# Optimization experiments

Hardware: AMD Instinct MI355X
Metric: run time of the kernel (lower is better)

Reference implementation:

```python
import jax, jax.numpy as jnp
import numpy as np

S, B, H = 2048, 4, 1024

def setup_inputs() -> dict:
    key = jax.random.key(0)
    ks = jax.random.split(key, 9)
    s = 1.0 / np.sqrt(H)
    return {
        "x": jax.random.normal(ks[0], (S, B, H), jnp.float32),
        "ssm": jax.random.normal(ks[1], (B, S, S), jnp.float32),
        "Wq": jax.random.uniform(ks[2], (H, H), jnp.float32, -s, s),
        "bq": jax.random.uniform(ks[3], (H,), jnp.float32, -s, s),
        "Wk": jax.random.uniform(ks[4], (H, H), jnp.float32, -s, s),
        "bk": jax.random.uniform(ks[5], (H,), jnp.float32, -s, s),
        "Wv": jax.random.uniform(ks[6], (H, H), jnp.float32, -s, s),
        "bv": jax.random.uniform(ks[7], (H,), jnp.float32, -s, s),
        "beta": jnp.array(1.0, jnp.float32),
    }

def reference(x, ssm, Wq, bq, Wk, bk, Wv, bv, beta):
    scale = x.shape[-1] ** 0.5
    # projections on [S,B,H], then move to [B,S,H]
    Q = jnp.einsum('sbh,oh->bso', x, Wq) + bq
    K = jnp.einsum('sbh,oh->bso', x, Wk) + bk
    V = jnp.einsum('sbh,oh->bso', x, Wv) + bv
    scores = jnp.einsum('bqh,bkh->bqk', Q, K) / scale + beta * ssm
    attn = jax.nn.softmax(scores, axis=-1)
    out = jnp.einsum('bqk,bkh->bqh', attn, V)  # [B,S,H]
    return out.transpose(1, 0, 2)  # [S,B,H]
```

## Files before the change

kernel.cpp:

```cpp
#include <hip/hip_runtime.h>
#include <stdint.h>


#define S_LEN 2048
#define BATCH 4
#define HDIM  1024

typedef unsigned short u16;
typedef float f32x4  __attribute__((ext_vector_type(4)));
typedef short bf16x8 __attribute__((ext_vector_type(8)));
typedef u16   u16x4  __attribute__((ext_vector_type(4)));

__device__ __forceinline__ u16 f2bf(float f) {
  union { float f; uint32_t u; } c; c.f = f;
  uint32_t u = c.u;
  u += 0x7fffu + ((u >> 16) & 1u);
  return (u16)(u >> 16);
}

__global__ __launch_bounds__(256) void cast_f32_bf16(const float* __restrict__ src,
                                                     u16* __restrict__ dst, int n4) {
  int i = blockIdx.x * 256 + threadIdx.x;
  if (i >= n4) return;
  f32x4 v = *(const f32x4*)(src + (size_t)i * 4);
  u16x4 o;
  o.x = f2bf(v.x); o.y = f2bf(v.y); o.z = f2bf(v.z); o.w = f2bf(v.w);
  *(u16x4*)(dst + (size_t)i * 4) = o;
}

template <int MODE>
__global__ __launch_bounds__(256)
void gemm_bt(const u16* __restrict__ A, int lda, long bsA,
             const u16* __restrict__ Bm, int ldb, long bsB,
             void* __restrict__ Cp, int ldc, long bsC,
             int K,
             const float* __restrict__ E, int ldE, long bsE,
             const float* __restrict__ beta_p, float scale) {
  __shared__ u16 lA[128 * 64];
  __shared__ u16 lB[128 * 64];
  const int t = threadIdx.x;
  const int lane = t & 63;
  const int wave = t >> 6;
  const int wm = wave & 1, wn = wave >> 1;
  const int z = blockIdx.z;
  A  += (size_t)z * (size_t)bsA;
  Bm += (size_t)z * (size_t)bsB;
  const size_t brow = (size_t)blockIdx.x * 128;
  const size_t bcol = (size_t)blockIdx.y * 128;

  f32x4 acc[4][4] = {};

  int rowT[4], scT[4];
#pragma unroll
  for (int j = 0; j < 4; ++j) {
    int o = j * 4096 + t * 16;
    int row = o >> 7;
    int ch = (o >> 4) & 7;
    rowT[j] = row;
    scT[j] = (ch ^ (row & 7)) * 8;
  }
  const int ldsw = wave * 512;

  const u16* pA[4];
  const u16* pB[4];
#pragma unroll
  for (int j = 0; j < 4; ++j) {
    pA[j] = A  + (brow + rowT[j]) * (size_t)lda + scT[j];
    pB[j] = Bm + (bcol + rowT[j]) * (size_t)ldb + scT[j];
  }

  int offA[2][4], offB[2][4];
#pragma unroll
  for (int ks = 0; ks < 2; ++ks) {
#pragma unroll
    for (int i = 0; i < 4; ++i) {
      int ra = wm * 64 + i * 16 + (lane & 15);
      int rb = wn * 64 + i * 16 + (lane & 15);
      int c = ks * 4 + (lane >> 4);
      offA[ks][i] = ra * 64 + ((c ^ (ra & 7)) * 8);
      offB[ks][i] = rb * 64 + ((c ^ (rb & 7)) * 8);
    }
  }

  for (int k0 = 0; k0 < K; k0 += 64) {
    if (k0) __syncthreads();
#pragma unroll
    for (int j = 0; j < 4; ++j)
      __builtin_amdgcn_global_load_lds(
          (const __attribute__((address_space(1))) void*)(pA[j] + k0),
          (__attribute__((address_space(3))) void*)(lA + j * 2048 + ldsw), 16, 0, 0);
#pragma unroll
    for (int j = 0; j < 4; ++j)
      __builtin_amdgcn_global_load_lds(
          (const __attribute__((address_space(1))) void*)(pB[j] + k0),
          (__attribute__((address_space(3))) void*)(lB + j * 2048 + ldsw), 16, 0, 0);
    __syncthreads();

#pragma unroll
    for (int ks = 0; ks < 2; ++ks) {
      bf16x8 af[4], bf_[4];
#pragma unroll
      for (int mi = 0; mi < 4; ++mi) af[mi] = *(const bf16x8*)(lA + offA[ks][mi]);
#pragma unroll
      for (int ni = 0; ni < 4; ++ni) bf_[ni] = *(const bf16x8*)(lB + offB[ks][ni]);
#pragma unroll
      for (int mi = 0; mi < 4; ++mi)
#pragma unroll
        for (int ni = 0; ni < 4; ++ni)
          acc[mi][ni] = __builtin_amdgcn_mfma_f32_16x16x32_bf16(af[mi], bf_[ni],
                                                                acc[mi][ni], 0, 0, 0);
    }
  }

  const int r0 = (int)brow + wm * 64 + ((lane >> 4) << 2);
  const int c0 = (int)bcol + wn * 64 + (lane & 15);
  if constexpr (MODE == 0) {
    u16* C = (u16*)Cp;
#pragma unroll
    for (int ni = 0; ni < 4; ++ni) {
      int cc = c0 + ni * 16;
      float bv = E[cc];
#pragma unroll
      for (int mi = 0; mi < 4; ++mi)
#pragma unroll
        for (int q = 0; q < 4; ++q)
          C[(size_t)(r0 + mi * 16 + q) * ldc + cc] = f2bf((acc[mi][ni][q] + bv) * scale);
    }
  } else if constexpr (MODE == 1) {
    float* C = (float*)Cp + (size_t)z * (size_t)bsC;
    const float* Ez = E + (size_t)z * (size_t)bsE;
    const float beta = *beta_p;
#pragma unroll
    for (int ni = 0; ni < 4; ++ni) {
      int cc = c0 + ni * 16;
#pragma unroll
      for (int mi = 0; mi < 4; ++mi)
#pragma unroll
        for (int q = 0; q < 4; ++q) {
          int rr = r0 + mi * 16 + q;
          C[(size_t)rr * ldc + cc] = acc[mi][ni][q] + beta * Ez[(size_t)rr * ldE + cc];
        }
    }
  } else {
    float* C = (float*)Cp + (size_t)z * (size_t)bsC;
#pragma unroll
    for (int ni = 0; ni < 4; ++ni) {
      int cc = c0 + ni * 16;
#pragma unroll
      for (int mi = 0; mi < 4; ++mi)
#pragma unroll
        for (int q = 0; q < 4; ++q)
          C[(size_t)(r0 + mi * 16 + q) * ldc + cc] = acc[mi][ni][q];
    }
  }
}

__global__ __launch_bounds__(256) void transpose_v(const u16* __restrict__ V,
                                                   u16* __restrict__ Vt) {
  __shared__ u16 tile[64][68];
  const int b = blockIdx.z;
  const int s0 = blockIdx.x << 6, h0 = blockIdx.y << 6;
  const int t = threadIdx.x;
#pragma unroll
  for (int i = 0; i < 4; ++i) {
    int sl = (t >> 4) + i * 16;
    int hq = (t & 15) << 2;
    u16x4 v = *(const u16x4*)&V[((size_t)(s0 + sl) * BATCH + b) * HDIM + h0 + hq];
    *(u16x4*)&tile[sl][hq] = v;
  }
  __syncthreads();
#pragma unroll
  for (int i = 0; i < 4; ++i) {
    int hl = (t >> 4) + i * 16;
    int sq = (t & 15) << 2;
    u16x4 v;
    v.x = tile[sq + 0][hl]; v.y = tile[sq + 1][hl];
    v.z = tile[sq + 2][hl]; v.w = tile[sq + 3][hl];
    *(u16x4*)&Vt[((size_t)b * HDIM + h0 + hl) * S_LEN + s0 + sq] = v;
  }
}

__global__ __launch_bounds__(256) void softmax_row(float* __restrict__ scores) {
  const size_t row = blockIdx.x;
  float* rp = scores + row * 2048;
  const int t = threadIdx.x;
  const int lane = t & 63, wave = t >> 6;
  f32x4 v0 = *(const f32x4*)(rp + t * 8);
  f32x4 v1 = *(const f32x4*)(rp + t * 8 + 4);
  float m = -3.0e38f;
#pragma unroll
  for (int i = 0; i < 4; ++i) m = fmaxf(m, fmaxf(v0[i], v1[i]));
#pragma unroll
  for (int off = 32; off > 0; off >>= 1) m = fmaxf(m, __shfl_xor(m, off));
  __shared__ float red[8];
  if (lane == 0) red[wave] = m;
  __syncthreads();
  m = fmaxf(fmaxf(red[0], red[1]), fmaxf(red[2], red[3]));
  float e[8], s = 0.f;
#pragma unroll
  for (int i = 0; i < 4; ++i) { e[i] = __expf(v0[i] - m); s += e[i]; }
#pragma unroll
  for (int i = 0; i < 4; ++i) { e[4 + i] = __expf(v1[i] - m); s += e[4 + i]; }
#pragma unroll
  for (int off = 32; off > 0; off >>= 1) s += __shfl_xor(s, off);
  if (lane == 0) red[4 + wave] = s;
  __syncthreads();
  s = (red[4] + red[5]) + (red[6] + red[7]);
  const float inv = 1.0f / s;
  u16* wp = (u16*)rp;
  u16x4 o0, o1;
  o0.x = f2bf(e[0] * inv); o0.y = f2bf(e[1] * inv);
  o0.z = f2bf(e[2] * inv); o0.w = f2bf(e[3] * inv);
  o1.x = f2bf(e[4] * inv); o1.y = f2bf(e[5] * inv);
  o1.z = f2bf(e[6] * inv); o1.w = f2bf(e[7] * inv);
  *(u16x4*)(wp + t * 8) = o0;
  *(u16x4*)(wp + t * 8 + 4) = o1;
}

extern "C" void kernel_launch(void* const* d_in, const int* in_sizes, int n_in,
                              void* d_out, int out_size, void* d_ws, size_t ws_size,
                              hipStream_t stream) {
  const float* x    = (const float*)d_in[0];
  const float* ssm  = (const float*)d_in[1];
  const float* Wq   = (const float*)d_in[2];
  const float* bq   = (const float*)d_in[3];
  const float* Wk   = (const float*)d_in[4];
  const float* bk   = (const float*)d_in[5];
  const float* Wv   = (const float*)d_in[6];
  const float* bv   = (const float*)d_in[7];
  const float* beta = (const float*)d_in[8];
  float* out = (float*)d_out;

  char* p = (char*)d_ws;
  u16* xb  = (u16*)p; p += (size_t)8192 * 1024 * 2;
  u16* wqb = (u16*)p; p += (size_t)1024 * 1024 * 2;
  u16* wkb = (u16*)p; p += (size_t)1024 * 1024 * 2;
  u16* wvb = (u16*)p; p += (size_t)1024 * 1024 * 2;
  u16* Qs  = (u16*)p; p += (size_t)8192 * 1024 * 2;
  u16* Kb  = (u16*)p; p += (size_t)8192 * 1024 * 2;
  u16* Vb  = (u16*)p; p += (size_t)8192 * 1024 * 2;
  u16* Vt  = (u16*)p; p += (size_t)BATCH * HDIM * S_LEN * 2;
  float* sc = (float*)p;

  cast_f32_bf16<<<8192, 256, 0, stream>>>(x, xb, 2097152);
  cast_f32_bf16<<<1024, 256, 0, stream>>>(Wq, wqb, 262144);
  cast_f32_bf16<<<1024, 256, 0, stream>>>(Wk, wkb, 262144);
  cast_f32_bf16<<<1024, 256, 0, stream>>>(Wv, wvb, 262144);

  dim3 gp(64, 8, 1);
  gemm_bt<0><<<gp, 256, 0, stream>>>(xb, 1024, 0, wqb, 1024, 0, Qs, 1024, 0, 1024,
                                     bq, 0, 0, nullptr, 0.03125f);
  gemm_bt<0><<<gp, 256, 0, stream>>>(xb, 1024, 0, wkb, 1024, 0, Kb, 1024, 0, 1024,
                                     bk, 0, 0, nullptr, 1.0f);
  gemm_bt<0><<<gp, 256, 0, stream>>>(xb, 1024, 0, wvb, 1024, 0, Vb, 1024, 0, 1024,
                                     bv, 0, 0, nullptr, 1.0f);

  transpose_v<<<dim3(32, 16, 4), 256, 0, stream>>>(Vb, Vt);

  dim3 gs(16, 16, 4);
  gemm_bt<1><<<gs, 256, 0, stream>>>(Qs, 4096, 1024, Kb, 4096, 1024,
                                     sc, 2048, (long)2048 * 2048, 1024,
                                     ssm, 2048, (long)2048 * 2048, beta, 1.0f);

  softmax_row<<<8192, 256, 0, stream>>>(sc);

  dim3 gv(16, 8, 4);
  gemm_bt<2><<<gv, 256, 0, stream>>>((const u16*)sc, 4096, 8388608,
                                     Vt, 2048, (long)HDIM * S_LEN,
                                     out, 4096, 1024, 2048,
                                     nullptr, 0, 0, nullptr, 1.0f);
}
```

Before: 333.5 us.

## Fuse QKV projections into one 256x256-tile pipelined GEMM and reuse it for scores

Concatenates Wq/Wk/Wv and the biases so a single GEMM produces an interleaved QKV buffer. It adds a new 256x256-tile, 512-thread GEMM that double-buffers LDS and splits each k-step into four MFMA quadrants with barriers and raised priority, overlapping global-to-LDS loads with compute. The same kernel computes the scores GEMM, with the 1/sqrt(H) scale moved from the Q projection to the epilogue. The aim is fewer launches, more data reuse per tile and better load/compute overlap, at the cost of 128KB of LDS per block and a fragile hand-written wait/barrier schedule.

After: 383.2 us. +14.9%, slower.

```diff
diff --git a/kernel.cpp b/kernel.cpp
--- a/kernel.cpp
+++ b/kernel.cpp
@@ -26,6 +26,149 @@
   u16x4 o;
   o.x = f2bf(v.x); o.y = f2bf(v.y); o.z = f2bf(v.z); o.w = f2bf(v.w);
   *(u16x4*)(dst + (size_t)i * 4) = o;
+}
+
+__global__ __launch_bounds__(256) void pack_bias(const float* __restrict__ bq,
+                                                 const float* __restrict__ bk,
+                                                 const float* __restrict__ bv,
+                                                 float* __restrict__ bb) {
+  int i = blockIdx.x * 256 + threadIdx.x;
+  if (i < 1024) bb[i] = bq[i];
+  else if (i < 2048) bb[i] = bk[i - 1024];
+  else if (i < 3072) bb[i] = bv[i - 2048];
+}
+
+#define AS1 __attribute__((address_space(1)))
+#define AS3 __attribute__((address_space(3)))
+
+template <int MODE>
+__global__ __launch_bounds__(512, 2)
+void gemm256(const u16* __restrict__ A, int lda, long bsA,
+             const u16* __restrict__ Bm, int ldb, long bsB,
+             void* __restrict__ Cp, int ldc, long bsC,
+             int K,
+             const float* __restrict__ E, int ldE, long bsE,
+             const float* __restrict__ beta_p, float scale) {
+  __shared__ u16 lds[65536];
+  const int t = threadIdx.x;
+  const int lane = t & 63, wave = t >> 6;
+  const int wm = wave >> 2, wn = wave & 3;
+  const int z = blockIdx.z;
+  A  += (size_t)z * (size_t)bsA;
+  Bm += (size_t)z * (size_t)bsB;
+  const size_t brow = (size_t)blockIdx.x * 256;
+  const size_t bcol = (size_t)blockIdx.y * 256;
+  const int NT = K >> 6;
+
+  const int l8 = lane >> 3, l7 = lane & 7;
+  const int srow = wave * 8 + l8;
+  const int scol = (l7 ^ l8) * 8;
+  const u16* gA = A  + (size_t)(brow + srow) * lda + scol;
+  const u16* gB = Bm + (size_t)(bcol + srow) * ldb + scol;
+
+  const int fr = lane & 15, fc = lane >> 4;
+  int roff[2];
+  roff[0] = fr * 64 + ((0 * 4 + fc) ^ l7) * 8;
+  roff[1] = fr * 64 + ((1 * 4 + fc) ^ l7) * 8;
+
+  f32x4 acc[8][4] = {};
+  bf16x8 Af[4][2];
+  bf16x8 Bf[2][2][2];
+
+#define STAGE_A(kt, buf, q) __builtin_amdgcn_global_load_lds( \
+    (const AS1 void*)(gA + (size_t)(q) * 64 * lda + (size_t)(kt) * 64), \
+    (AS3 void*)(lds + (buf) * 32768 + (q) * 4096 + wave * 512), 16, 0, 0)
+#define STAGE_B(kt, buf, q) __builtin_amdgcn_global_load_lds( \
+    (const AS1 void*)(gB + (size_t)(q) * 64 * ldb + (size_t)(kt) * 64), \
+    (AS3 void*)(lds + (buf) * 32768 + 16384 + (q) * 4096 + wave * 512), 16, 0, 0)
+#define READ_A(mh) { _Pragma("unroll") for (int mi = 0; mi < 4; ++mi) { \
+    _Pragma("unroll") for (int ks = 0; ks < 2; ++ks) \
+      Af[mi][ks] = *(const bf16x8*)(LA + (wm * 128 + (mh) * 64 + mi * 16) * 64 + roff[ks]); } }
+#define READ_B(nh) { _Pragma("unroll") for (int ni = 0; ni < 2; ++ni) { \
+    _Pragma("unroll") for (int ks = 0; ks < 2; ++ks) \
+      Bf[nh][ni][ks] = *(const bf16x8*)(LB + (wn * 64 + (nh) * 32 + ni * 16) * 64 + roff[ks]); } }
+#define MFMA_Q(mh, nh) { _Pragma("unroll") for (int mi = 0; mi < 4; ++mi) { \
+    _Pragma("unroll") for (int ni = 0; ni < 2; ++ni) { \
+      _Pragma("unroll") for (int ks = 0; ks < 2; ++ks) \
+        acc[(mh) * 4 + mi][(nh) * 2 + ni] = __builtin_amdgcn_mfma_f32_16x16x32_bf16( \
+            Af[mi][ks], Bf[nh][ni][ks], acc[(mh) * 4 + mi][(nh) * 2 + ni], 0, 0, 0); } } }
+#define BAR() __builtin_amdgcn_s_barrier()
+#define LGKM0() asm volatile("s_waitcnt lgkmcnt(0)" ::: "memory")
+
+#pragma unroll
+  for (int q = 0; q < 4; ++q) STAGE_A(0, 0, q);
+#pragma unroll
+  for (int q = 0; q < 4; ++q) STAGE_B(0, 0, q);
+  STAGE_A(1, 1, 0); STAGE_A(1, 1, 2); STAGE_B(1, 1, 0); STAGE_B(1, 1, 1);
+  asm volatile("s_waitcnt vmcnt(4)" ::: "memory");
+  BAR();
+
+  int cur = 0;
+  for (int kt = 0; kt < NT; ++kt) {
+    const u16* LA = lds + cur * 32768;
+    const u16* LB = LA + 16384;
+    const int nxt = cur ^ 1;
+    READ_A(0); READ_B(0);
+    if (kt + 1 < NT) { STAGE_A(kt + 1, nxt, 1); STAGE_A(kt + 1, nxt, 3);
+                       STAGE_B(kt + 1, nxt, 2); STAGE_B(kt + 1, nxt, 3); }
+    BAR(); LGKM0();
+    __builtin_amdgcn_s_setprio(1); MFMA_Q(0, 0); __builtin_amdgcn_s_setprio(0);
+    BAR();
+    READ_B(1);
+    BAR(); LGKM0();
+    __builtin_amdgcn_s_setprio(1); MFMA_Q(0, 1); __builtin_amdgcn_s_setprio(0);
+    BAR();
+    READ_A(1);
+    if (kt + 2 < NT) { STAGE_A(kt + 2, cur, 0); STAGE_A(kt + 2, cur, 2); }
+    BAR(); LGKM0();
+    __builtin_amdgcn_s_setprio(1); MFMA_Q(1, 0); __builtin_amdgcn_s_setprio(0);
+    BAR();
+    if (kt + 2 < NT) { STAGE_B(kt + 2, cur, 0); STAGE_B(kt + 2, cur, 1); }
+    BAR(); LGKM0();
+    __builtin_amdgcn_s_setprio(1); MFMA_Q(1, 1); __builtin_amdgcn_s_setprio(0);
+    if (kt + 2 < NT) { asm volatile("s_waitcnt vmcnt(4)" ::: "memory"); }
+    else             { asm volatile("s_waitcnt vmcnt(0)" ::: "memory"); }
+    BAR();
+    cur = nxt;
+  }
+
+  const int r0 = (int)brow + wm * 128 + fc * 4;
+  const int c0 = (int)bcol + wn * 64 + fr;
+  if constexpr (MODE == 0) {
+    u16* C = (u16*)Cp;
+#pragma unroll
+    for (int nf = 0; nf < 4; ++nf) {
+      int cc = c0 + nf * 16;
+      float bv = E[cc];
+#pragma unroll
+      for (int mf = 0; mf < 8; ++mf)
+#pragma unroll
+        for (int q = 0; q < 4; ++q)
+          C[(size_t)(r0 + mf * 16 + q) * ldc + cc] = f2bf(acc[mf][nf][q] + bv);
+    }
+  } else {
+    float* C = (float*)Cp + (size_t)z * (size_t)bsC;
+    const float* Ez = E + (size_t)z * (size_t)bsE;
+    const float beta = *beta_p;
+#pragma unroll
+    for (int nf = 0; nf < 4; ++nf) {
+      int cc = c0 + nf * 16;
+#pragma unroll
+      for (int mf = 0; mf < 8; ++mf)
+#pragma unroll
+        for (int q = 0; q < 4; ++q) {
+          int rr = r0 + mf * 16 + q;
+          C[(size_t)rr * ldc + cc] = acc[mf][nf][q] * scale + beta * Ez[(size_t)rr * ldE + cc];
+        }
+    }
+  }
+#undef STAGE_A
+#undef STAGE_B
+#undef READ_A
+#undef READ_B
+#undef MFMA_Q
+#undef BAR
+#undef LGKM0
 }
 
 template <int MODE>
@@ -87,13 +230,13 @@
 #pragma unroll
     for (int j = 0; j < 4; ++j)
       __builtin_amdgcn_global_load_lds(
-          (const __attribute__((address_space(1))) void*)(pA[j] + k0),
-          (__attribute__((address_space(3))) void*)(lA + j * 2048 + ldsw), 16, 0, 0);
+          (const AS1 void*)(pA[j] + k0),
+          (AS3 void*)(lA + j * 2048 + ldsw), 16, 0, 0);
 #pragma unroll
     for (int j = 0; j < 4; ++j)
       __builtin_amdgcn_global_load_lds(
-          (const __attribute__((address_space(1))) void*)(pB[j] + k0),
-          (__attribute__((address_space(3))) void*)(lB + j * 2048 + ldsw), 16, 0, 0);
+          (const AS1 void*)(pB[j] + k0),
+          (AS3 void*)(lB + j * 2048 + ldsw), 16, 0, 0);
     __syncthreads();
 
 #pragma unroll
@@ -114,38 +257,11 @@
 
   const int r0 = (int)brow + wm * 64 + ((lane >> 4) << 2);
   const int c0 = (int)bcol + wn * 64 + (lane & 15);
-  if constexpr (MODE == 0) {
-    u16* C = (u16*)Cp;
+  {
+    float* C = (float*)Cp + (size_t)z * (size_t)bsC;
 #pragma unroll
     for (int ni = 0; ni < 4; ++ni) {
       int cc = c0 + ni * 16;
-      float bv = E[cc];
-#pragma unroll
-      for (int mi = 0; mi < 4; ++mi)
-#pragma unroll
-        for (int q = 0; q < 4; ++q)
-          C[(size_t)(r0 + mi * 16 + q) * ldc + cc] = f2bf((acc[mi][ni][q] + bv) * scale);
-    }
-  } else if constexpr (MODE == 1) {
-    float* C = (float*)Cp + (size_t)z * (size_t)bsC;
-    const float* Ez = E + (size_t)z * (size_t)bsE;
-    const float beta = *beta_p;
-#pragma unroll
-    for (int ni = 0; ni < 4; ++ni) {
-      int cc = c0 + ni * 16;
-#pragma unroll
-      for (int mi = 0; mi < 4; ++mi)
-#pragma unroll
-        for (int q = 0; q < 4; ++q) {
-          int rr = r0 + mi * 16 + q;
-          C[(size_t)rr * ldc + cc] = acc[mi][ni][q] + beta * Ez[(size_t)rr * ldE + cc];
-        }
-    }
-  } else {
-    float* C = (float*)Cp + (size_t)z * (size_t)bsC;
-#pragma unroll
-    for (int ni = 0; ni < 4; ++ni) {
-      int cc = c0 + ni * 16;
 #pragma unroll
       for (int mi = 0; mi < 4; ++mi)
 #pragma unroll
@@ -155,7 +271,7 @@
   }
 }
 
-__global__ __launch_bounds__(256) void transpose_v(const u16* __restrict__ V,
+__global__ __launch_bounds__(256) void transpose_v(const u16* __restrict__ QKV,
                                                    u16* __restrict__ Vt) {
   __shared__ u16 tile[64][68];
   const int b = blockIdx.z;
@@ -165,7 +281,7 @@
   for (int i = 0; i < 4; ++i) {
     int sl = (t >> 4) + i * 16;
     int hq = (t & 15) << 2;
-    u16x4 v = *(const u16x4*)&V[((size_t)(s0 + sl) * BATCH + b) * HDIM + h0 + hq];
+    u16x4 v = *(const u16x4*)&QKV[((size_t)(s0 + sl) * BATCH + b) * 3072 + 2048 + h0 + hq];
     *(u16x4*)&tile[sl][hq] = v;
   }
   __syncthreads();
@@ -233,34 +349,29 @@
 
   char* p = (char*)d_ws;
   u16* xb  = (u16*)p; p += (size_t)8192 * 1024 * 2;
-  u16* wqb = (u16*)p; p += (size_t)1024 * 1024 * 2;
-  u16* wkb = (u16*)p; p += (size_t)1024 * 1024 * 2;
-  u16* wvb = (u16*)p; p += (size_t)1024 * 1024 * 2;
-  u16* Qs  = (u16*)p; p += (size_t)8192 * 1024 * 2;
-  u16* Kb  = (u16*)p; p += (size_t)8192 * 1024 * 2;
-  u16* Vb  = (u16*)p; p += (size_t)8192 * 1024 * 2;
+  u16* wb  = (u16*)p; p += (size_t)3072 * 1024 * 2;
+  float* bb = (float*)p; p += 3072 * 4;
+  u16* QKV = (u16*)p; p += (size_t)8192 * 3072 * 2;
   u16* Vt  = (u16*)p; p += (size_t)BATCH * HDIM * S_LEN * 2;
   float* sc = (float*)p;
 
   cast_f32_bf16<<<8192, 256, 0, stream>>>(x, xb, 2097152);
-  cast_f32_bf16<<<1024, 256, 0, stream>>>(Wq, wqb, 262144);
-  cast_f32_bf16<<<1024, 256, 0, stream>>>(Wk, wkb, 262144);
-  cast_f32_bf16<<<1024, 256, 0, stream>>>(Wv, wvb, 262144);
-
-  dim3 gp(64, 8, 1);
-  gemm_bt<0><<<gp, 256, 0, stream>>>(xb, 1024, 0, wqb, 1024, 0, Qs, 1024, 0, 1024,
-                                     bq, 0, 0, nullptr, 0.03125f);
-  gemm_bt<0><<<gp, 256, 0, stream>>>(xb, 1024, 0, wkb, 1024, 0, Kb, 1024, 0, 1024,
-                                     bk, 0, 0, nullptr, 1.0f);
-  gemm_bt<0><<<gp, 256, 0, stream>>>(xb, 1024, 0, wvb, 1024, 0, Vb, 1024, 0, 1024,
-                                     bv, 0, 0, nullptr, 1.0f);
-
-  transpose_v<<<dim3(32, 16, 4), 256, 0, stream>>>(Vb, Vt);
-
-  dim3 gs(16, 16, 4);
-  gemm_bt<1><<<gs, 256, 0, stream>>>(Qs, 4096, 1024, Kb, 4096, 1024,
-                                     sc, 2048, (long)2048 * 2048, 1024,
-                                     ssm, 2048, (long)2048 * 2048, beta, 1.0f);
+  cast_f32_bf16<<<1024, 256, 0, stream>>>(Wq, wb, 262144);
+  cast_f32_bf16<<<1024, 256, 0, stream>>>(Wk, wb + 1024 * 1024, 262144);
+  cast_f32_bf16<<<1024, 256, 0, stream>>>(Wv, wb + 2048 * 1024, 262144);
+  pack_bias<<<12, 256, 0, stream>>>(bq, bk, bv, bb);
+
+  gemm256<0><<<dim3(32, 12, 1), 512, 0, stream>>>(xb, 1024, 0, wb, 1024, 0,
+                                                  QKV, 3072, 0, 1024,
+                                                  bb, 0, 0, nullptr, 1.0f);
+
+  transpose_v<<<dim3(32, 16, 4), 256, 0, stream>>>(QKV, Vt);
+
+  gemm256<1><<<dim3(8, 8, 4), 512, 0, stream>>>(QKV, 12288, 3072,
+                                                QKV + 1024, 12288, 3072,
+                                                sc, 2048, (long)2048 * 2048, 1024,
+                                                ssm, 2048, (long)2048 * 2048,
+                                                beta, 0.03125f);
 
   softmax_row<<<8192, 256, 0, stream>>>(sc);
 
```

## Fuse QKV projections into one GEMM, merge casts, add XCD-aware block remap

Applied to the files above, without the earlier changes.

Merges the four cast kernels into one launch that also packs the biases, and concatenates Wq/Wk/Wv so a single GEMM writes an interleaved QKV buffer. The Q scaling moves from the projection epilogue into the scores epilogue. All GEMMs now use a 1D grid with a swizzle that spreads consecutive tiles across the eight XCDs for better L2 locality. This cuts launch count and gives one larger projection GEMM, at the cost of a wider stride (3072) in the later reads of Q, K and V.

Result: slower. 341.6 us (+2.4%).

```diff
diff --git a/kernel.cpp b/kernel.cpp
--- a/kernel.cpp
+++ b/kernel.cpp
@@ -10,6 +10,9 @@
 typedef float f32x4  __attribute__((ext_vector_type(4)));
 typedef short bf16x8 __attribute__((ext_vector_type(8)));
 typedef u16   u16x4  __attribute__((ext_vector_type(4)));
+
+#define AS1 __attribute__((address_space(1)))
+#define AS3 __attribute__((address_space(3)))
 
 __device__ __forceinline__ u16 f2bf(float f) {
   union { float f; uint32_t u; } c; c.f = f;
@@ -18,14 +21,31 @@
   return (u16)(u >> 16);
 }
 
-__global__ __launch_bounds__(256) void cast_f32_bf16(const float* __restrict__ src,
-                                                     u16* __restrict__ dst, int n4) {
+__global__ __launch_bounds__(256)
+void cast_all(const float* __restrict__ x,
+              const float* __restrict__ Wq, const float* __restrict__ Wk,
+              const float* __restrict__ Wv,
+              const float* __restrict__ bq, const float* __restrict__ bk,
+              const float* __restrict__ bv,
+              u16* __restrict__ xb, u16* __restrict__ wb, float* __restrict__ bb) {
   int i = blockIdx.x * 256 + threadIdx.x;
-  if (i >= n4) return;
-  f32x4 v = *(const f32x4*)(src + (size_t)i * 4);
+  const float* src;
+  u16* dst;
+  if (i < 2097152) { src = x + (size_t)i * 4; dst = xb + (size_t)i * 4; }
+  else if (i < 2359296) { int j = i - 2097152; src = Wq + (size_t)j * 4; dst = wb + (size_t)j * 4; }
+  else if (i < 2621440) { int j = i - 2359296; src = Wk + (size_t)j * 4; dst = wb + 1048576 + (size_t)j * 4; }
+  else if (i < 2883584) { int j = i - 2621440; src = Wv + (size_t)j * 4; dst = wb + 2097152 + (size_t)j * 4; }
+  else {
+    int j = i - 2883584;
+    const float* s = (j < 256) ? bq : (j < 512) ? bk : bv;
+    int o = ((j < 256) ? j : (j < 512) ? j - 256 : j - 512) * 4;
+    *(f32x4*)(bb + j * 4) = *(const f32x4*)(s + o);
+    return;
+  }
+  f32x4 v = *(const f32x4*)src;
   u16x4 o;
   o.x = f2bf(v.x); o.y = f2bf(v.y); o.z = f2bf(v.z); o.w = f2bf(v.w);
-  *(u16x4*)(dst + (size_t)i * 4) = o;
+  *(u16x4*)dst = o;
 }
 
 template <int MODE>
@@ -35,18 +55,25 @@
              void* __restrict__ Cp, int ldc, long bsC,
              int K,
              const float* __restrict__ E, int ldE, long bsE,
-             const float* __restrict__ beta_p, float scale) {
+             const float* __restrict__ beta_p, float scale,
+             int gx, int gy) {
   __shared__ u16 lA[128 * 64];
   __shared__ u16 lB[128 * 64];
   const int t = threadIdx.x;
   const int lane = t & 63;
   const int wave = t >> 6;
   const int wm = wave & 1, wn = wave >> 1;
-  const int z = blockIdx.z;
-  A  += (size_t)z * (size_t)bsA;
-  Bm += (size_t)z * (size_t)bsB;
-  const size_t brow = (size_t)blockIdx.x * 128;
-  const size_t bcol = (size_t)blockIdx.y * 128;
+  const int nwg = gridDim.x;
+  const int w = ((blockIdx.x & 7) * (nwg >> 3)) + (blockIdx.x >> 3);
+  const int pp = gx * gy;
+  const int bz = w / pp;
+  const int rem = w - bz * pp;
+  const int by = rem / gx;
+  const int bx = rem - by * gx;
+  A  += (size_t)bz * (size_t)bsA;
+  Bm += (size_t)bz * (size_t)bsB;
+  const size_t brow = (size_t)bx * 128;
+  const size_t bcol = (size_t)by * 128;
 
   f32x4 acc[4][4] = {};
 
@@ -87,13 +114,13 @@
 #pragma unroll
     for (int j = 0; j < 4; ++j)
       __builtin_amdgcn_global_load_lds(
-          (const __attribute__((address_space(1))) void*)(pA[j] + k0),
-          (__attribute__((address_space(3))) void*)(lA + j * 2048 + ldsw), 16, 0, 0);
+          (const AS1 void*)(pA[j] + k0),
+          (AS3 void*)(lA + j * 2048 + ldsw), 16, 0, 0);
 #pragma unroll
     for (int j = 0; j < 4; ++j)
       __builtin_amdgcn_global_load_lds(
-          (const __attribute__((address_space(1))) void*)(pB[j] + k0),
-          (__attribute__((address_space(3))) void*)(lB + j * 2048 + ldsw), 16, 0, 0);
+          (const AS1 void*)(pB[j] + k0),
+          (AS3 void*)(lB + j * 2048 + ldsw), 16, 0, 0);
     __syncthreads();
 
 #pragma unroll
@@ -127,8 +154,8 @@
           C[(size_t)(r0 + mi * 16 + q) * ldc + cc] = f2bf((acc[mi][ni][q] + bv) * scale);
     }
   } else if constexpr (MODE == 1) {
-    float* C = (float*)Cp + (size_t)z * (size_t)bsC;
-    const float* Ez = E + (size_t)z * (size_t)bsE;
+    float* C = (float*)Cp + (size_t)bz * (size_t)bsC;
+    const float* Ez = E + (size_t)bz * (size_t)bsE;
     const float beta = *beta_p;
 #pragma unroll
     for (int ni = 0; ni < 4; ++ni) {
@@ -138,11 +165,11 @@
 #pragma unroll
         for (int q = 0; q < 4; ++q) {
           int rr = r0 + mi * 16 + q;
-          C[(size_t)rr * ldc + cc] = acc[mi][ni][q] + beta * Ez[(size_t)rr * ldE + cc];
+          C[(size_t)rr * ldc + cc] = acc[mi][ni][q] * scale + beta * Ez[(size_t)rr * ldE + cc];
         }
     }
   } else {
-    float* C = (float*)Cp + (size_t)z * (size_t)bsC;
+    float* C = (float*)Cp + (size_t)bz * (size_t)bsC;
 #pragma unroll
     for (int ni = 0; ni < 4; ++ni) {
       int cc = c0 + ni * 16;
@@ -155,7 +182,7 @@
   }
 }
 
-__global__ __launch_bounds__(256) void transpose_v(const u16* __restrict__ V,
+__global__ __launch_bounds__(256) void transpose_v(const u16* __restrict__ QKV,
                                                    u16* __restrict__ Vt) {
   __shared__ u16 tile[64][68];
   const int b = blockIdx.z;
@@ -165,7 +192,7 @@
   for (int i = 0; i < 4; ++i) {
     int sl = (t >> 4) + i * 16;
     int hq = (t & 15) << 2;
-    u16x4 v = *(const u16x4*)&V[((size_t)(s0 + sl) * BATCH + b) * HDIM + h0 + hq];
+    u16x4 v = *(const u16x4*)&QKV[((size_t)(s0 + sl) * BATCH + b) * 3072 + 2048 + h0 + hq];
     *(u16x4*)&tile[sl][hq] = v;
   }
   __syncthreads();
@@ -233,40 +260,30 @@
 
   char* p = (char*)d_ws;
   u16* xb  = (u16*)p; p += (size_t)8192 * 1024 * 2;
-  u16* wqb = (u16*)p; p += (size_t)1024 * 1024 * 2;
-  u16* wkb = (u16*)p; p += (size_t)1024 * 1024 * 2;
-  u16* wvb = (u16*)p; p += (size_t)1024 * 1024 * 2;
-  u16* Qs  = (u16*)p; p += (size_t)8192 * 1024 * 2;
-  u16* Kb  = (u16*)p; p += (size_t)8192 * 1024 * 2;
-  u16* Vb  = (u16*)p; p += (size_t)8192 * 1024 * 2;
+  u16* wb  = (u16*)p; p += (size_t)3072 * 1024 * 2;
+  float* bb = (float*)p; p += 3072 * 4;
+  u16* QKV = (u16*)p; p += (size_t)8192 * 3072 * 2;
   u16* Vt  = (u16*)p; p += (size_t)BATCH * HDIM * S_LEN * 2;
   float* sc = (float*)p;
 
-  cast_f32_bf16<<<8192, 256, 0, stream>>>(x, xb, 2097152);
-  cast_f32_bf16<<<1024, 256, 0, stream>>>(Wq, wqb, 262144);
-  cast_f32_bf16<<<1024, 256, 0, stream>>>(Wk, wkb, 262144);
-  cast_f32_bf16<<<1024, 256, 0, stream>>>(Wv, wvb, 262144);
-
-  dim3 gp(64, 8, 1);
-  gemm_bt<0><<<gp, 256, 0, stream>>>(xb, 1024, 0, wqb, 1024, 0, Qs, 1024, 0, 1024,
-                                     bq, 0, 0, nullptr, 0.03125f);
-  gemm_bt<0><<<gp, 256, 0, stream>>>(xb, 1024, 0, wkb, 1024, 0, Kb, 1024, 0, 1024,
-                                     bk, 0, 0, nullptr, 1.0f);
-  gemm_bt<0><<<gp, 256, 0, stream>>>(xb, 1024, 0, wvb, 1024, 0, Vb, 1024, 0, 1024,
-                                     bv, 0, 0, nullptr, 1.0f);
-
-  transpose_v<<<dim3(32, 16, 4), 256, 0, stream>>>(Vb, Vt);
-
-  dim3 gs(16, 16, 4);
-  gemm_bt<1><<<gs, 256, 0, stream>>>(Qs, 4096, 1024, Kb, 4096, 1024,
-                                     sc, 2048, (long)2048 * 2048, 1024,
-                                     ssm, 2048, (long)2048 * 2048, beta, 1.0f);
+  cast_all<<<11267, 256, 0, stream>>>(x, Wq, Wk, Wv, bq, bk, bv, xb, wb, bb);
+
+  gemm_bt<0><<<1536, 256, 0, stream>>>(xb, 1024, 0, wb, 1024, 0,
+                                       QKV, 3072, 0, 1024,
+                                       bb, 0, 0, nullptr, 1.0f, 64, 24);
+
+  transpose_v<<<dim3(32, 16, 4), 256, 0, stream>>>(QKV, Vt);
+
+  gemm_bt<1><<<1024, 256, 0, stream>>>(QKV, 12288, 3072,
+                                       QKV + 1024, 12288, 3072,
+                                       sc, 2048, (long)2048 * 2048, 1024,
+                                       ssm, 2048, (long)2048 * 2048,
+                                       beta, 0.03125f, 16, 16);
 
   softmax_row<<<8192, 256, 0, stream>>>(sc);
 
-  dim3 gv(16, 8, 4);
-  gemm_bt<2><<<gv, 256, 0, stream>>>((const u16*)sc, 4096, 8388608,
-                                     Vt, 2048, (long)HDIM * S_LEN,
-                                     out, 4096, 1024, 2048,
-                                     nullptr, 0, 0, nullptr, 1.0f);
-}
+  gemm_bt<2><<<512, 256, 0, stream>>>((const u16*)sc, 4096, 8388608,
+                                      Vt, 2048, (long)HDIM * S_LEN,
+                                      out, 4096, 1024, 2048,
+                                      nullptr, 0, 0, nullptr, 1.0f, 16, 8);
+}
```
